# Optimization experiments

Measured on AMD Instinct MI355X. Metric: run time of the kernel, lower is better.

The kernel has to match this reference:

```python
import jax, jax.numpy as jnp
import numpy as np

TEMPERATURE = 1.0

def _logic_layer(x, sel_a, sel_b, gate_logits, temp):
    # x: [B, in], sel_a/sel_b: [n, in], gate_logits: [n, 16]
    a = jax.nn.softmax(sel_a / temp, axis=-1)
    b = jax.nn.softmax(sel_b / temp, axis=-1)
    p = jnp.einsum('bi,ni->bn', x, a)  # first soft operand  [B, n]
    q = jnp.einsum('bi,ni->bn', x, b)  # second soft operand [B, n]
    pq = p * q
    one = jnp.ones_like(p)
    zero = jnp.zeros_like(p)
    # 16 two-input probabilistic logic gates (difflogic ordering)
    gates = jnp.stack([
        zero,               # FALSE
        pq,                 # AND
        p - pq,             # A AND NOT B
        p,                  # A
        q - pq,             # NOT A AND B
        q,                  # B
        p + q - 2 * pq,     # XOR
        p + q - pq,         # OR
        one - (p + q - pq), # NOR
        one - (p + q - 2 * pq),  # XNOR
        one - q,            # NOT B
        one - q + pq,       # A OR NOT B
        one - p,            # NOT A
        one - p + pq,       # NOT A OR B
        one - pq,           # NAND
        one,                # TRUE
    ], axis=-1)  # [B, n, 16]
    w = jax.nn.softmax(gate_logits / temp, axis=-1)  # [n, 16]
    return jnp.einsum('bng,ng->bn', gates, w)


def setup_inputs() -> dict:
    key = jax.random.key(0)
    ks = jax.random.split(key, 13)
    B = 1048576  # 1024x1024 CA grid, flattened cells
    inp = {'x': jax.random.uniform(ks[0], (B, 9), dtype=jnp.float32)}
    dims = [(8, 9), (4, 8), (2, 4), (1, 2)]
    i = 1
    for li, (n, d) in enumerate(dims, start=1):
        inp[f'sa{li}'] = jax.random.normal(ks[i], (n, d), dtype=jnp.float32); i += 1
        inp[f'sb{li}'] = jax.random.normal(ks[i], (n, d), dtype=jnp.float32); i += 1
        inp[f'g{li}'] = jax.random.normal(ks[i], (n, 16), dtype=jnp.float32); i += 1
    return inp


def reference(x, sa1, sb1, g1, sa2, sb2, g2, sa3, sb3, g3, sa4, sb4, g4):
    t = TEMPERATURE
    h = _logic_layer(x, sa1, sb1, g1, t)   # [B, 8]
    h = _logic_layer(h, sa2, sb2, g2, t)   # [B, 4]
    h = _logic_layer(h, sa3, sb3, g3, t)   # [B, 2]
    h = _logic_layer(h, sa4, sb4, g4, t)   # [B, 1]
    return h
```

## Files before the change

### kernel.cpp

```cpp
#include <hip/hip_runtime.h>
#include <math.h>


#define THREADS 256
#define SPT 4
#define B_PER_BLOCK (THREADS * SPT)

__global__ void coeff_kernel(const float* sa1, const float* sb1, const float* g1,
                             const float* sa2, const float* sb2, const float* g2,
                             const float* sa3, const float* sb3, const float* g3,
                             const float* sa4, const float* sb4, const float* g4,
                             float* cf) {
    int t = threadIdx.x;
    const float k0[16]  = {0,0,0,0, 0,0,0,0, 1, 1, 1, 1, 1, 1, 1, 1};
    const float kp[16]  = {0,0,1,1, 0,0,1,1,-1,-1, 0, 0,-1,-1, 0, 0};
    const float kq[16]  = {0,0,0,0, 1,1,1,1,-1,-1,-1,-1, 0, 0, 0, 0};
    const float kpq[16] = {0,1,-1,0,-1,0,-2,-1, 1, 2, 0, 1, 0, 1,-1, 0};

    const float *sa, *sb, *g;
    float *A, *Bc, *C;
    int d;
    if (t < 8)       { int j = t;      d = 9; sa = sa1 + j*9; sb = sb1 + j*9; g = g1 + j*16; A = cf       + j*9; Bc = cf +  72 + j*9; C = cf + 144 + j*4; }
    else if (t < 12) { int j = t - 8;  d = 8; sa = sa2 + j*8; sb = sb2 + j*8; g = g2 + j*16; A = cf + 176 + j*8; Bc = cf + 208 + j*8; C = cf + 240 + j*4; }
    else if (t < 14) { int j = t - 12; d = 4; sa = sa3 + j*4; sb = sb3 + j*4; g = g3 + j*16; A = cf + 256 + j*4; Bc = cf + 264 + j*4; C = cf + 272 + j*4; }
    else if (t == 14){                 d = 2; sa = sa4;       sb = sb4;       g = g4;        A = cf + 280;       Bc = cf + 282;       C = cf + 284; }
    else return;

    {
        float m = -1e30f;
        for (int i = 0; i < d; ++i) m = fmaxf(m, sa[i]);
        float e[9], s = 0.f;
        for (int i = 0; i < d; ++i) { e[i] = expf(sa[i] - m); s += e[i]; }
        for (int i = 0; i < d; ++i) A[i] = e[i] / s;
    }
    {
        float m = -1e30f;
        for (int i = 0; i < d; ++i) m = fmaxf(m, sb[i]);
        float e[9], s = 0.f;
        for (int i = 0; i < d; ++i) { e[i] = expf(sb[i] - m); s += e[i]; }
        for (int i = 0; i < d; ++i) Bc[i] = e[i] / s;
    }
    {
        float m = -1e30f;
        for (int i = 0; i < 16; ++i) m = fmaxf(m, g[i]);
        float w[16], s = 0.f;
        for (int i = 0; i < 16; ++i) { w[i] = expf(g[i] - m); s += w[i]; }
        float c0 = 0, c1 = 0, c2 = 0, c3 = 0;
        for (int i = 0; i < 16; ++i) {
            float wi = w[i] / s;
            c0 += wi * k0[i]; c1 += wi * kp[i]; c2 += wi * kq[i]; c3 += wi * kpq[i];
        }
        C[0] = c0; C[1] = c1; C[2] = c2; C[3] = c3;
    }
}

__global__ __launch_bounds__(THREADS) void net_kernel(
        const float* __restrict__ x, const float* __restrict__ cf,
        float* __restrict__ out, int nB) {
    __shared__ float sx[B_PER_BLOCK * 9];
    const int t = threadIdx.x;
    const int blockBase = blockIdx.x * B_PER_BLOCK;
    const int total = nB * 9;
    const int f4base = blockBase * 9 / 4;

    const float4* __restrict__ x4 = (const float4*)x;
    float4* sx4 = (float4*)sx;
    #pragma unroll
    for (int k = 0; k < 9; ++k) {
        int fi = f4base + t + k * 256;
        int e  = fi * 4;
        if (e + 3 < total) {
            sx4[t + k * 256] = x4[fi];
        } else {
            float4 vv = {0.f, 0.f, 0.f, 0.f};
            if (e     < total) vv.x = x[e];
            if (e + 1 < total) vv.y = x[e + 1];
            if (e + 2 < total) vv.z = x[e + 2];
            sx4[t + k * 256] = vv;
        }
    }
    __syncthreads();

    float v[SPT][9];
    #pragma unroll
    for (int s = 0; s < SPT; ++s) {
        const int r = s * THREADS + t;
        #pragma unroll
        for (int i = 0; i < 9; ++i) v[s][i] = sx[r * 9 + i];
    }

    float h1[SPT][8];
    #pragma unroll
    for (int j = 0; j < 8; ++j) {
        float A[9], Bv[9], C[4];
        #pragma unroll
        for (int i = 0; i < 9; ++i) { A[i] = cf[j * 9 + i]; Bv[i] = cf[72 + j * 9 + i]; }
        #pragma unroll
        for (int c = 0; c < 4; ++c) C[c] = cf[144 + j * 4 + c];
        #pragma unroll
        for (int s = 0; s < SPT; ++s) {
            float p = 0.f, q = 0.f;
            #pragma unroll
            for (int i = 0; i < 9; ++i) { p = fmaf(v[s][i], A[i], p); q = fmaf(v[s][i], Bv[i], q); }
            h1[s][j] = fmaf(C[3], p * q, fmaf(C[2], q, fmaf(C[1], p, C[0])));
        }
    }
    float h2[SPT][4];
    #pragma unroll
    for (int j = 0; j < 4; ++j) {
        float A[8], Bv[8], C[4];
        #pragma unroll
        for (int i = 0; i < 8; ++i) { A[i] = cf[176 + j * 8 + i]; Bv[i] = cf[208 + j * 8 + i]; }
        #pragma unroll
        for (int c = 0; c < 4; ++c) C[c] = cf[240 + j * 4 + c];
        #pragma unroll
        for (int s = 0; s < SPT; ++s) {
            float p = 0.f, q = 0.f;
            #pragma unroll
            for (int i = 0; i < 8; ++i) { p = fmaf(h1[s][i], A[i], p); q = fmaf(h1[s][i], Bv[i], q); }
            h2[s][j] = fmaf(C[3], p * q, fmaf(C[2], q, fmaf(C[1], p, C[0])));
        }
    }
    float h3[SPT][2];
    #pragma unroll
    for (int j = 0; j < 2; ++j) {
        float A[4], Bv[4], C[4];
        #pragma unroll
        for (int i = 0; i < 4; ++i) { A[i] = cf[256 + j * 4 + i]; Bv[i] = cf[264 + j * 4 + i]; }
        #pragma unroll
        for (int c = 0; c < 4; ++c) C[c] = cf[272 + j * 4 + c];
        #pragma unroll
        for (int s = 0; s < SPT; ++s) {
            float p = 0.f, q = 0.f;
            #pragma unroll
            for (int i = 0; i < 4; ++i) { p = fmaf(h2[s][i], A[i], p); q = fmaf(h2[s][i], Bv[i], q); }
            h3[s][j] = fmaf(C[3], p * q, fmaf(C[2], q, fmaf(C[1], p, C[0])));
        }
    }
    {
        float a0 = cf[280], a1 = cf[281], b0 = cf[282], b1 = cf[283];
        float c0 = cf[284], c1 = cf[285], c2 = cf[286], c3 = cf[287];
        #pragma unroll
        for (int s = 0; s < SPT; ++s) {
            float p = fmaf(h3[s][0], a0, h3[s][1] * a1);
            float q = fmaf(h3[s][0], b0, h3[s][1] * b1);
            float o = fmaf(c3, p * q, fmaf(c2, q, fmaf(c1, p, c0)));
            int b = blockBase + s * THREADS + t;
            if (b < nB) out[b] = o;
        }
    }
}

extern "C" void kernel_launch(void* const* d_in, const int* in_sizes, int n_in,
                              void* d_out, int out_size, void* d_ws, size_t ws_size,
                              hipStream_t stream) {
    const float* x   = (const float*)d_in[0];
    const float* sa1 = (const float*)d_in[1];
    const float* sb1 = (const float*)d_in[2];
    const float* g1  = (const float*)d_in[3];
    const float* sa2 = (const float*)d_in[4];
    const float* sb2 = (const float*)d_in[5];
    const float* g2  = (const float*)d_in[6];
    const float* sa3 = (const float*)d_in[7];
    const float* sb3 = (const float*)d_in[8];
    const float* g3  = (const float*)d_in[9];
    const float* sa4 = (const float*)d_in[10];
    const float* sb4 = (const float*)d_in[11];
    const float* g4  = (const float*)d_in[12];
    float* cf = (float*)d_ws;
    const int nB = in_sizes[0] / 9;

    coeff_kernel<<<1, 64, 0, stream>>>(sa1, sb1, g1, sa2, sb2, g2,
                                       sa3, sb3, g3, sa4, sb4, g4, cf);
    const int grid = (nB + B_PER_BLOCK - 1) / B_PER_BLOCK;
    net_kernel<<<grid, THREADS, 0, stream>>>(x, cf, (float*)d_out, nB);
}
```

Measured before the change: 129.8 us.

## Fuse coefficient softmax into net kernel with warp-specialized loading

```diff
diff --git a/kernel.cpp b/kernel.cpp
--- a/kernel.cpp
+++ b/kernel.cpp
@@ -6,77 +6,81 @@
 #define SPT 4
 #define B_PER_BLOCK (THREADS * SPT)
 
-__global__ void coeff_kernel(const float* sa1, const float* sb1, const float* g1,
-                             const float* sa2, const float* sb2, const float* g2,
-                             const float* sa3, const float* sb3, const float* g3,
-                             const float* sa4, const float* sb4, const float* g4,
-                             float* cf) {
-    int t = threadIdx.x;
-    const float k0[16]  = {0,0,0,0, 0,0,0,0, 1, 1, 1, 1, 1, 1, 1, 1};
-    const float kp[16]  = {0,0,1,1, 0,0,1,1,-1,-1, 0, 0,-1,-1, 0, 0};
-    const float kq[16]  = {0,0,0,0, 1,1,1,1,-1,-1,-1,-1, 0, 0, 0, 0};
-    const float kpq[16] = {0,1,-1,0,-1,0,-2,-1, 1, 2, 0, 1, 0, 1,-1, 0};
+__global__ __launch_bounds__(THREADS) void fused_net_kernel(
+        const float* __restrict__ x,
+        const float* __restrict__ sa1, const float* __restrict__ sb1, const float* __restrict__ g1,
+        const float* __restrict__ sa2, const float* __restrict__ sb2, const float* __restrict__ g2,
+        const float* __restrict__ sa3, const float* __restrict__ sb3, const float* __restrict__ g3,
+        const float* __restrict__ sa4, const float* __restrict__ sb4, const float* __restrict__ g4,
+        float* __restrict__ out, int nB) {
+    __shared__ float scf[288];
+    __shared__ float sx[B_PER_BLOCK * 9];
 
-    const float *sa, *sb, *g;
-    float *A, *Bc, *C;
-    int d;
-    if (t < 8)       { int j = t;      d = 9; sa = sa1 + j*9; sb = sb1 + j*9; g = g1 + j*16; A = cf       + j*9; Bc = cf +  72 + j*9; C = cf + 144 + j*4; }
-    else if (t < 12) { int j = t - 8;  d = 8; sa = sa2 + j*8; sb = sb2 + j*8; g = g2 + j*16; A = cf + 176 + j*8; Bc = cf + 208 + j*8; C = cf + 240 + j*4; }
-    else if (t < 14) { int j = t - 12; d = 4; sa = sa3 + j*4; sb = sb3 + j*4; g = g3 + j*16; A = cf + 256 + j*4; Bc = cf + 264 + j*4; C = cf + 272 + j*4; }
-    else if (t == 14){                 d = 2; sa = sa4;       sb = sb4;       g = g4;        A = cf + 280;       Bc = cf + 282;       C = cf + 284; }
-    else return;
-
-    {
-        float m = -1e30f;
-        for (int i = 0; i < d; ++i) m = fmaxf(m, sa[i]);
-        float e[9], s = 0.f;
-        for (int i = 0; i < d; ++i) { e[i] = expf(sa[i] - m); s += e[i]; }
-        for (int i = 0; i < d; ++i) A[i] = e[i] / s;
-    }
-    {
-        float m = -1e30f;
-        for (int i = 0; i < d; ++i) m = fmaxf(m, sb[i]);
-        float e[9], s = 0.f;
-        for (int i = 0; i < d; ++i) { e[i] = expf(sb[i] - m); s += e[i]; }
-        for (int i = 0; i < d; ++i) Bc[i] = e[i] / s;
-    }
-    {
-        float m = -1e30f;
-        for (int i = 0; i < 16; ++i) m = fmaxf(m, g[i]);
-        float w[16], s = 0.f;
-        for (int i = 0; i < 16; ++i) { w[i] = expf(g[i] - m); s += w[i]; }
-        float c0 = 0, c1 = 0, c2 = 0, c3 = 0;
-        for (int i = 0; i < 16; ++i) {
-            float wi = w[i] / s;
-            c0 += wi * k0[i]; c1 += wi * kp[i]; c2 += wi * kq[i]; c3 += wi * kpq[i];
-        }
-        C[0] = c0; C[1] = c1; C[2] = c2; C[3] = c3;
-    }
-}
-
-__global__ __launch_bounds__(THREADS) void net_kernel(
-        const float* __restrict__ x, const float* __restrict__ cf,
-        float* __restrict__ out, int nB) {
-    __shared__ float sx[B_PER_BLOCK * 9];
     const int t = threadIdx.x;
     const int blockBase = blockIdx.x * B_PER_BLOCK;
     const int total = nB * 9;
-    const int f4base = blockBase * 9 / 4;
 
-    const float4* __restrict__ x4 = (const float4*)x;
-    float4* sx4 = (float4*)sx;
-    #pragma unroll
-    for (int k = 0; k < 9; ++k) {
-        int fi = f4base + t + k * 256;
-        int e  = fi * 4;
-        if (e + 3 < total) {
-            sx4[t + k * 256] = x4[fi];
-        } else {
-            float4 vv = {0.f, 0.f, 0.f, 0.f};
-            if (e     < total) vv.x = x[e];
-            if (e + 1 < total) vv.y = x[e + 1];
-            if (e + 2 < total) vv.z = x[e + 2];
-            sx4[t + k * 256] = vv;
+    if (t < 64) {
+        if (t < 15) {
+            const float k0[16]  = {0,0,0,0, 0,0,0,0, 1, 1, 1, 1, 1, 1, 1, 1};
+            const float kp[16]  = {0,0,1,1, 0,0,1,1,-1,-1, 0, 0,-1,-1, 0, 0};
+            const float kq[16]  = {0,0,0,0, 1,1,1,1,-1,-1,-1,-1, 0, 0, 0, 0};
+            const float kpq[16] = {0,1,-1,0,-1,0,-2,-1, 1, 2, 0, 1, 0, 1,-1, 0};
+
+            const float *sa, *sb, *g;
+            float *A, *Bc, *C;
+            int d;
+            if (t < 8)       { int j = t;      d = 9; sa = sa1 + j*9; sb = sb1 + j*9; g = g1 + j*16; A = scf       + j*9; Bc = scf +  72 + j*9; C = scf + 144 + j*4; }
+            else if (t < 12) { int j = t - 8;  d = 8; sa = sa2 + j*8; sb = sb2 + j*8; g = g2 + j*16; A = scf + 176 + j*8; Bc = scf + 208 + j*8; C = scf + 240 + j*4; }
+            else if (t < 14) { int j = t - 12; d = 4; sa = sa3 + j*4; sb = sb3 + j*4; g = g3 + j*16; A = scf + 256 + j*4; Bc = scf + 264 + j*4; C = scf + 272 + j*4; }
+            else             {                 d = 2; sa = sa4;       sb = sb4;       g = g4;        A = scf + 280;       Bc = scf + 282;       C = scf + 284; }
+
+            {
+                float m = -1e30f;
+                for (int i = 0; i < d; ++i) m = fmaxf(m, sa[i]);
+                float e[9], s = 0.f;
+                for (int i = 0; i < d; ++i) { e[i] = expf(sa[i] - m); s += e[i]; }
+                for (int i = 0; i < d; ++i) A[i] = e[i] / s;
+            }
+            {
+                float m = -1e30f;
+                for (int i = 0; i < d; ++i) m = fmaxf(m, sb[i]);
+                float e[9], s = 0.f;
+                for (int i = 0; i < d; ++i) { e[i] = expf(sb[i] - m); s += e[i]; }
+                for (int i = 0; i < d; ++i) Bc[i] = e[i] / s;
+            }
+            {
+                float m = -1e30f;
+                for (int i = 0; i < 16; ++i) m = fmaxf(m, g[i]);
+                float w[16], s = 0.f;
+                for (int i = 0; i < 16; ++i) { w[i] = expf(g[i] - m); s += w[i]; }
+                float c0 = 0, c1 = 0, c2 = 0, c3 = 0;
+                for (int i = 0; i < 16; ++i) {
+                    float wi = w[i] / s;
+                    c0 += wi * k0[i]; c1 += wi * kp[i]; c2 += wi * kq[i]; c3 += wi * kpq[i];
+                }
+                C[0] = c0; C[1] = c1; C[2] = c2; C[3] = c3;
+            }
+        }
+    } else {
+        const int tt = t - 64;
+        const int f4base = blockBase * 9 / 4;
+        const float4* __restrict__ x4 = (const float4*)x;
+        float4* sx4 = (float4*)sx;
+        #pragma unroll
+        for (int k = 0; k < 12; ++k) {
+            int idx = tt + k * 192;
+            int fi  = f4base + idx;
+            int e   = fi * 4;
+            if (e + 3 < total) {
+                sx4[idx] = x4[fi];
+            } else {
+                float4 vv = {0.f, 0.f, 0.f, 0.f};
+                if (e     < total) vv.x = x[e];
+                if (e + 1 < total) vv.y = x[e + 1];
+                if (e + 2 < total) vv.z = x[e + 2];
+                sx4[idx] = vv;
+            }
         }
     }
     __syncthreads();
@@ -88,58 +92,62 @@
         #pragma unroll
         for (int i = 0; i < 9; ++i) v[s][i] = sx[r * 9 + i];
     }
+    asm volatile("" ::: "memory");
 
     float h1[SPT][8];
     #pragma unroll
     for (int j = 0; j < 8; ++j) {
-        float A[9], Bv[9], C[4];
+        float A[9], Bv[9], C4[4];
         #pragma unroll
-        for (int i = 0; i < 9; ++i) { A[i] = cf[j * 9 + i]; Bv[i] = cf[72 + j * 9 + i]; }
+        for (int i = 0; i < 9; ++i) { A[i] = scf[j * 9 + i]; Bv[i] = scf[72 + j * 9 + i]; }
         #pragma unroll
-        for (int c = 0; c < 4; ++c) C[c] = cf[144 + j * 4 + c];
+        for (int c = 0; c < 4; ++c) C4[c] = scf[144 + j * 4 + c];
         #pragma unroll
         for (int s = 0; s < SPT; ++s) {
             float p = 0.f, q = 0.f;
             #pragma unroll
             for (int i = 0; i < 9; ++i) { p = fmaf(v[s][i], A[i], p); q = fmaf(v[s][i], Bv[i], q); }
-            h1[s][j] = fmaf(C[3], p * q, fmaf(C[2], q, fmaf(C[1], p, C[0])));
+            h1[s][j] = fmaf(C4[3], p * q, fmaf(C4[2], q, fmaf(C4[1], p, C4[0])));
         }
+        asm volatile("" ::: "memory");
     }
     float h2[SPT][4];
     #pragma unroll
     for (int j = 0; j < 4; ++j) {
-        float A[8], Bv[8], C[4];
+        float A[8], Bv[8], C4[4];
         #pragma unroll
-        for (int i = 0; i < 8; ++i) { A[i] = cf[176 + j * 8 + i]; Bv[i] = cf[208 + j * 8 + i]; }
+        for (int i = 0; i < 8; ++i) { A[i] = scf[176 + j * 8 + i]; Bv[i] = scf[208 + j * 8 + i]; }
         #pragma unroll
-        for (int c = 0; c < 4; ++c) C[c] = cf[240 + j * 4 + c];
+        for (int c = 0; c < 4; ++c) C4[c] = scf[240 + j * 4 + c];
         #pragma unroll
         for (int s = 0; s < SPT; ++s) {
             float p = 0.f, q = 0.f;
             #pragma unroll
             for (int i = 0; i < 8; ++i) { p = fmaf(h1[s][i], A[i], p); q = fmaf(h1[s][i], Bv[i], q); }
-            h2[s][j] = fmaf(C[3], p * q, fmaf(C[2], q, fmaf(C[1], p, C[0])));
+            h2[s][j] = fmaf(C4[3], p * q, fmaf(C4[2], q, fmaf(C4[1], p, C4[0])));
         }
+        asm volatile("" ::: "memory");
     }
     float h3[SPT][2];
     #pragma unroll
     for (int j = 0; j < 2; ++j) {
-        float A[4], Bv[4], C[4];
+        float A[4], Bv[4], C4[4];
         #pragma unroll
-        for (int i = 0; i < 4; ++i) { A[i] = cf[256 + j * 4 + i]; Bv[i] = cf[264 + j * 4 + i]; }
+        for (int i = 0; i < 4; ++i) { A[i] = scf[256 + j * 4 + i]; Bv[i] = scf[264 + j * 4 + i]; }
         #pragma unroll
-        for (int c = 0; c < 4; ++c) C[c] = cf[272 + j * 4 + c];
+        for (int c = 0; c < 4; ++c) C4[c] = scf[272 + j * 4 + c];
         #pragma unroll
         for (int s = 0; s < SPT; ++s) {
             float p = 0.f, q = 0.f;
             #pragma unroll
             for (int i = 0; i < 4; ++i) { p = fmaf(h2[s][i], A[i], p); q = fmaf(h2[s][i], Bv[i], q); }
-            h3[s][j] = fmaf(C[3], p * q, fmaf(C[2], q, fmaf(C[1], p, C[0])));
+            h3[s][j] = fmaf(C4[3], p * q, fmaf(C4[2], q, fmaf(C4[1], p, C4[0])));
         }
+        asm volatile("" ::: "memory");
     }
     {
-        float a0 = cf[280], a1 = cf[281], b0 = cf[282], b1 = cf[283];
-        float c0 = cf[284], c1 = cf[285], c2 = cf[286], c3 = cf[287];
+        float a0 = scf[280], a1 = scf[281], b0 = scf[282], b1 = scf[283];
+        float c0 = scf[284], c1 = scf[285], c2 = scf[286], c3 = scf[287];
         #pragma unroll
         for (int s = 0; s < SPT; ++s) {
             float p = fmaf(h3[s][0], a0, h3[s][1] * a1);
@@ -167,11 +175,10 @@
     const float* sa4 = (const float*)d_in[10];
     const float* sb4 = (const float*)d_in[11];
     const float* g4  = (const float*)d_in[12];
-    float* cf = (float*)d_ws;
     const int nB = in_sizes[0] / 9;
 
-    coeff_kernel<<<1, 64, 0, stream>>>(sa1, sb1, g1, sa2, sb2, g2,
-                                       sa3, sb3, g3, sa4, sb4, g4, cf);
     const int grid = (nB + B_PER_BLOCK - 1) / B_PER_BLOCK;
-    net_kernel<<<grid, THREADS, 0, stream>>>(x, cf, (float*)d_out, nB);
+    fused_net_kernel<<<grid, THREADS, 0, stream>>>(
+        x, sa1, sb1, g1, sa2, sb2, g2, sa3, sb3, g3, sa4, sb4, g4,
+        (float*)d_out, nB);
 }
```

Result: slower. 141.5 us (+9.0%).

## Load inputs directly per thread with float4, drop LDS staging, vectorize output

Applied to the files above, without the earlier changes.

```diff
diff --git a/kernel.cpp b/kernel.cpp
--- a/kernel.cpp
+++ b/kernel.cpp
@@ -6,148 +6,166 @@
 #define SPT 4
 #define B_PER_BLOCK (THREADS * SPT)
 
-__global__ void coeff_kernel(const float* sa1, const float* sb1, const float* g1,
-                             const float* sa2, const float* sb2, const float* g2,
-                             const float* sa3, const float* sb3, const float* g3,
-                             const float* sa4, const float* sb4, const float* g4,
-                             float* cf) {
-    int t = threadIdx.x;
+template <int D>
+__device__ __forceinline__ void softmax_row(const float* __restrict__ src,
+                                            float* __restrict__ dst) {
+    float e[D];
+    float m = src[0];
+    #pragma unroll
+    for (int i = 1; i < D; ++i) m = fmaxf(m, src[i]);
+    float s = 0.f;
+    #pragma unroll
+    for (int i = 0; i < D; ++i) { e[i] = __expf(src[i] - m); s += e[i]; }
+    float inv = 1.f / s;
+    #pragma unroll
+    for (int i = 0; i < D; ++i) dst[i] = e[i] * inv;
+}
+
+__device__ __forceinline__ void gate_fold(const float* __restrict__ g,
+                                          float* __restrict__ C) {
     const float k0[16]  = {0,0,0,0, 0,0,0,0, 1, 1, 1, 1, 1, 1, 1, 1};
     const float kp[16]  = {0,0,1,1, 0,0,1,1,-1,-1, 0, 0,-1,-1, 0, 0};
     const float kq[16]  = {0,0,0,0, 1,1,1,1,-1,-1,-1,-1, 0, 0, 0, 0};
     const float kpq[16] = {0,1,-1,0,-1,0,-2,-1, 1, 2, 0, 1, 0, 1,-1, 0};
+    float w[16];
+    float m = g[0];
+    #pragma unroll
+    for (int i = 1; i < 16; ++i) m = fmaxf(m, g[i]);
+    float s = 0.f;
+    #pragma unroll
+    for (int i = 0; i < 16; ++i) { w[i] = __expf(g[i] - m); s += w[i]; }
+    float inv = 1.f / s;
+    float c0 = 0, c1 = 0, c2 = 0, c3 = 0;
+    #pragma unroll
+    for (int i = 0; i < 16; ++i) {
+        float wi = w[i] * inv;
+        c0 = fmaf(wi, k0[i], c0); c1 = fmaf(wi, kp[i], c1);
+        c2 = fmaf(wi, kq[i], c2); c3 = fmaf(wi, kpq[i], c3);
+    }
+    C[0] = c0; C[1] = c1; C[2] = c2; C[3] = c3;
+}
 
-    const float *sa, *sb, *g;
-    float *A, *Bc, *C;
-    int d;
-    if (t < 8)       { int j = t;      d = 9; sa = sa1 + j*9; sb = sb1 + j*9; g = g1 + j*16; A = cf       + j*9; Bc = cf +  72 + j*9; C = cf + 144 + j*4; }
-    else if (t < 12) { int j = t - 8;  d = 8; sa = sa2 + j*8; sb = sb2 + j*8; g = g2 + j*16; A = cf + 176 + j*8; Bc = cf + 208 + j*8; C = cf + 240 + j*4; }
-    else if (t < 14) { int j = t - 12; d = 4; sa = sa3 + j*4; sb = sb3 + j*4; g = g3 + j*16; A = cf + 256 + j*4; Bc = cf + 264 + j*4; C = cf + 272 + j*4; }
-    else if (t == 14){                 d = 2; sa = sa4;       sb = sb4;       g = g4;        A = cf + 280;       Bc = cf + 282;       C = cf + 284; }
-    else return;
-
-    {
-        float m = -1e30f;
-        for (int i = 0; i < d; ++i) m = fmaxf(m, sa[i]);
-        float e[9], s = 0.f;
-        for (int i = 0; i < d; ++i) { e[i] = expf(sa[i] - m); s += e[i]; }
-        for (int i = 0; i < d; ++i) A[i] = e[i] / s;
-    }
-    {
-        float m = -1e30f;
-        for (int i = 0; i < d; ++i) m = fmaxf(m, sb[i]);
-        float e[9], s = 0.f;
-        for (int i = 0; i < d; ++i) { e[i] = expf(sb[i] - m); s += e[i]; }
-        for (int i = 0; i < d; ++i) Bc[i] = e[i] / s;
-    }
-    {
-        float m = -1e30f;
-        for (int i = 0; i < 16; ++i) m = fmaxf(m, g[i]);
-        float w[16], s = 0.f;
-        for (int i = 0; i < 16; ++i) { w[i] = expf(g[i] - m); s += w[i]; }
-        float c0 = 0, c1 = 0, c2 = 0, c3 = 0;
-        for (int i = 0; i < 16; ++i) {
-            float wi = w[i] / s;
-            c0 += wi * k0[i]; c1 += wi * kp[i]; c2 += wi * kq[i]; c3 += wi * kpq[i];
-        }
-        C[0] = c0; C[1] = c1; C[2] = c2; C[3] = c3;
+__global__ void coeff_kernel(const float* __restrict__ sa1, const float* __restrict__ sb1, const float* __restrict__ g1,
+                             const float* __restrict__ sa2, const float* __restrict__ sb2, const float* __restrict__ g2,
+                             const float* __restrict__ sa3, const float* __restrict__ sb3, const float* __restrict__ g3,
+                             const float* __restrict__ sa4, const float* __restrict__ sb4, const float* __restrict__ g4,
+                             float* __restrict__ cf) {
+    int t = threadIdx.x;
+    if (t < 8) {
+        int j = t;
+        softmax_row<9>(sa1 + j * 9, cf + j * 9);
+        softmax_row<9>(sb1 + j * 9, cf + 72 + j * 9);
+        gate_fold(g1 + j * 16, cf + 144 + j * 4);
+    } else if (t < 12) {
+        int j = t - 8;
+        softmax_row<8>(sa2 + j * 8, cf + 176 + j * 8);
+        softmax_row<8>(sb2 + j * 8, cf + 208 + j * 8);
+        gate_fold(g2 + j * 16, cf + 240 + j * 4);
+    } else if (t < 14) {
+        int j = t - 12;
+        softmax_row<4>(sa3 + j * 4, cf + 256 + j * 4);
+        softmax_row<4>(sb3 + j * 4, cf + 264 + j * 4);
+        gate_fold(g3 + j * 16, cf + 272 + j * 4);
+    } else if (t == 14) {
+        softmax_row<2>(sa4, cf + 280);
+        softmax_row<2>(sb4, cf + 282);
+        gate_fold(g4, cf + 284);
     }
 }
 
-__global__ __launch_bounds__(THREADS) void net_kernel(
+__global__ __launch_bounds__(THREADS, 3) void net_kernel(
         const float* __restrict__ x, const float* __restrict__ cf,
         float* __restrict__ out, int nB) {
-    __shared__ float sx[B_PER_BLOCK * 9];
-    const int t = threadIdx.x;
-    const int blockBase = blockIdx.x * B_PER_BLOCK;
-    const int total = nB * 9;
-    const int f4base = blockBase * 9 / 4;
-
-    const float4* __restrict__ x4 = (const float4*)x;
-    float4* sx4 = (float4*)sx;
-    #pragma unroll
-    for (int k = 0; k < 9; ++k) {
-        int fi = f4base + t + k * 256;
-        int e  = fi * 4;
-        if (e + 3 < total) {
-            sx4[t + k * 256] = x4[fi];
-        } else {
-            float4 vv = {0.f, 0.f, 0.f, 0.f};
-            if (e     < total) vv.x = x[e];
-            if (e + 1 < total) vv.y = x[e + 1];
-            if (e + 2 < total) vv.z = x[e + 2];
-            sx4[t + k * 256] = vv;
-        }
-    }
-    __syncthreads();
+    const int T  = blockIdx.x * THREADS + threadIdx.x;
+    const int b0 = T * SPT;
+    if (b0 >= nB) return;
 
     float v[SPT][9];
-    #pragma unroll
-    for (int s = 0; s < SPT; ++s) {
-        const int r = s * THREADS + t;
+    if (b0 + SPT <= nB) {
+        const float4* __restrict__ x4 = (const float4*)x;
+        float4 r[9];
         #pragma unroll
-        for (int i = 0; i < 9; ++i) v[s][i] = sx[r * 9 + i];
+        for (int k = 0; k < 9; ++k) r[k] = x4[(long)T * 9 + k];
+        const float* rf = (const float*)r;
+        #pragma unroll
+        for (int s = 0; s < SPT; ++s)
+            #pragma unroll
+            for (int i = 0; i < 9; ++i) v[s][i] = rf[s * 9 + i];
+    } else {
+        #pragma unroll
+        for (int s = 0; s < SPT; ++s)
+            #pragma unroll
+            for (int i = 0; i < 9; ++i) {
+                int b = b0 + s;
+                v[s][i] = (b < nB) ? x[(long)b * 9 + i] : 0.f;
+            }
     }
 
     float h1[SPT][8];
     #pragma unroll
     for (int j = 0; j < 8; ++j) {
-        float A[9], Bv[9], C[4];
-        #pragma unroll
-        for (int i = 0; i < 9; ++i) { A[i] = cf[j * 9 + i]; Bv[i] = cf[72 + j * 9 + i]; }
-        #pragma unroll
-        for (int c = 0; c < 4; ++c) C[c] = cf[144 + j * 4 + c];
         #pragma unroll
         for (int s = 0; s < SPT; ++s) {
             float p = 0.f, q = 0.f;
             #pragma unroll
-            for (int i = 0; i < 9; ++i) { p = fmaf(v[s][i], A[i], p); q = fmaf(v[s][i], Bv[i], q); }
-            h1[s][j] = fmaf(C[3], p * q, fmaf(C[2], q, fmaf(C[1], p, C[0])));
+            for (int i = 0; i < 9; ++i) {
+                p = fmaf(v[s][i], cf[     j * 9 + i], p);
+                q = fmaf(v[s][i], cf[72 + j * 9 + i], q);
+            }
+            h1[s][j] = fmaf(cf[144 + j*4 + 3], p * q,
+                       fmaf(cf[144 + j*4 + 2], q,
+                       fmaf(cf[144 + j*4 + 1], p, cf[144 + j*4 + 0])));
         }
     }
     float h2[SPT][4];
     #pragma unroll
     for (int j = 0; j < 4; ++j) {
-        float A[8], Bv[8], C[4];
-        #pragma unroll
-        for (int i = 0; i < 8; ++i) { A[i] = cf[176 + j * 8 + i]; Bv[i] = cf[208 + j * 8 + i]; }
-        #pragma unroll
-        for (int c = 0; c < 4; ++c) C[c] = cf[240 + j * 4 + c];
         #pragma unroll
         for (int s = 0; s < SPT; ++s) {
             float p = 0.f, q = 0.f;
             #pragma unroll
-            for (int i = 0; i < 8; ++i) { p = fmaf(h1[s][i], A[i], p); q = fmaf(h1[s][i], Bv[i], q); }
-            h2[s][j] = fmaf(C[3], p * q, fmaf(C[2], q, fmaf(C[1], p, C[0])));
+            for (int i = 0; i < 8; ++i) {
+                p = fmaf(h1[s][i], cf[176 + j * 8 + i], p);
+                q = fmaf(h1[s][i], cf[208 + j * 8 + i], q);
+            }
+            h2[s][j] = fmaf(cf[240 + j*4 + 3], p * q,
+                       fmaf(cf[240 + j*4 + 2], q,
+                       fmaf(cf[240 + j*4 + 1], p, cf[240 + j*4 + 0])));
         }
     }
     float h3[SPT][2];
     #pragma unroll
     for (int j = 0; j < 2; ++j) {
-        float A[4], Bv[4], C[4];
-        #pragma unroll
-        for (int i = 0; i < 4; ++i) { A[i] = cf[256 + j * 4 + i]; Bv[i] = cf[264 + j * 4 + i]; }
-        #pragma unroll
-        for (int c = 0; c < 4; ++c) C[c] = cf[272 + j * 4 + c];
         #pragma unroll
         for (int s = 0; s < SPT; ++s) {
             float p = 0.f, q = 0.f;
             #pragma unroll
-            for (int i = 0; i < 4; ++i) { p = fmaf(h2[s][i], A[i], p); q = fmaf(h2[s][i], Bv[i], q); }
-            h3[s][j] = fmaf(C[3], p * q, fmaf(C[2], q, fmaf(C[1], p, C[0])));
+            for (int i = 0; i < 4; ++i) {
+                p = fmaf(h2[s][i], cf[256 + j * 4 + i], p);
+                q = fmaf(h2[s][i], cf[264 + j * 4 + i], q);
+            }
+            h3[s][j] = fmaf(cf[272 + j*4 + 3], p * q,
+                       fmaf(cf[272 + j*4 + 2], q,
+                       fmaf(cf[272 + j*4 + 1], p, cf[272 + j*4 + 0])));
         }
     }
-    {
-        float a0 = cf[280], a1 = cf[281], b0 = cf[282], b1 = cf[283];
-        float c0 = cf[284], c1 = cf[285], c2 = cf[286], c3 = cf[287];
+    float o[SPT];
+    #pragma unroll
+    for (int s = 0; s < SPT; ++s) {
+        float p = fmaf(h3[s][0], cf[280], h3[s][1] * cf[281]);
+        float q = fmaf(h3[s][0], cf[282], h3[s][1] * cf[283]);
+        o[s] = fmaf(cf[287], p * q,
+               fmaf(cf[286], q,
+               fmaf(cf[285], p, cf[284])));
+    }
+    if (b0 + SPT <= nB) {
+        float4* __restrict__ out4 = (float4*)out;
+        float4 w; w.x = o[0]; w.y = o[1]; w.z = o[2]; w.w = o[3];
+        out4[T] = w;
+    } else {
         #pragma unroll
-        for (int s = 0; s < SPT; ++s) {
-            float p = fmaf(h3[s][0], a0, h3[s][1] * a1);
-            float q = fmaf(h3[s][0], b0, h3[s][1] * b1);
-            float o = fmaf(c3, p * q, fmaf(c2, q, fmaf(c1, p, c0)));
-            int b = blockBase + s * THREADS + t;
-            if (b < nB) out[b] = o;
-        }
+        for (int s = 0; s < SPT; ++s)
+            if (b0 + s < nB) out[b0 + s] = o[s];
     }
 }
 
```

After: 107.6 us. 1.21x faster.
